# Optimization experiments

Hardware: AMD Instinct MI355X
Metric: run time of the kernel (lower is better)

The kernel has to match this reference:

```python
import jax, jax.numpy as jnp
import numpy as np

NUM_HEADS = 8
NUM_KV_HEADS = 2
HEAD_DIM = 64
EPS = 1e-6
ROPE_BASE = 10000.0


def rmsnorm(x, w):
    # x: (..., head_dim)
    var = jnp.mean(x * x, axis=-1, keepdims=True)
    return x * jax.lax.rsqrt(var + EPS) * w


def apply_rope(x):
    # x: (B, L, nH, hd); positions along L, standard rotate-half RoPE
    B, L, nH, hd = x.shape
    inv_freq = 1.0 / (ROPE_BASE ** (jnp.arange(0, hd, 2, dtype=jnp.float32) / hd))  # (hd/2,)
    ang = jnp.arange(L, dtype=jnp.float32)[:, None] * inv_freq[None, :]  # (L, hd/2)
    cos = jnp.concatenate([jnp.cos(ang), jnp.cos(ang)], axis=-1)[None, :, None, :]  # (1,L,1,hd)
    sin = jnp.concatenate([jnp.sin(ang), jnp.sin(ang)], axis=-1)[None, :, None, :]
    x1, x2 = jnp.split(x, 2, axis=-1)
    rot = jnp.concatenate([-x2, x1], axis=-1)
    return x * cos + rot * sin


def setup_inputs() -> dict:
    key = jax.random.key(0)
    ks = jax.random.split(key, 6)
    width = 512
    x = jax.random.normal(ks[0], (1, 16, 16, 16, width), dtype=jnp.float32)
    s = 1.0 / np.sqrt(width)
    Wq = jax.random.normal(ks[1], (width, width), dtype=jnp.float32) * s
    Wk = jax.random.normal(ks[2], (NUM_KV_HEADS * HEAD_DIM, width), dtype=jnp.float32) * s
    Wv = jax.random.normal(ks[3], (NUM_KV_HEADS * HEAD_DIM, width), dtype=jnp.float32) * s
    Wo = jax.random.normal(ks[4], (width, width), dtype=jnp.float32) * s
    q_norm_w = jnp.ones((HEAD_DIM,), dtype=jnp.float32)
    k_norm_w = jnp.ones((HEAD_DIM,), dtype=jnp.float32)
    return {"x": x, "Wq": Wq, "Wk": Wk, "Wv": Wv,
            "q_norm_w": q_norm_w, "k_norm_w": k_norm_w, "Wo": Wo}


def reference(x, Wq, Wk, Wv, q_norm_w, k_norm_w, Wo):
    B, H, W, D, C = x.shape
    L = H * W * D
    xf = x.reshape(B, L, C)
    q = (xf @ Wq.T).reshape(B, L, NUM_HEADS, HEAD_DIM)
    k = (xf @ Wk.T).reshape(B, L, NUM_KV_HEADS, HEAD_DIM)
    v = (xf @ Wv.T).reshape(B, L, NUM_KV_HEADS, HEAD_DIM)
    q = apply_rope(rmsnorm(q, q_norm_w))
    k = apply_rope(rmsnorm(k, k_norm_w))
    # (B, heads, L, hd)
    q = q.transpose(0, 2, 1, 3)
    k = k.transpose(0, 2, 1, 3)
    v = v.transpose(0, 2, 1, 3)
    repeats = NUM_HEADS // NUM_KV_HEADS
    if repeats > 1:
        k = jnp.repeat(k, repeats, axis=1)
        v = jnp.repeat(v, repeats, axis=1)
    scale = 1.0 / np.sqrt(HEAD_DIM)
    scores = jnp.einsum('bhqd,bhkd->bhqk', q, k) * scale
    attn = jax.nn.softmax(scores, axis=-1)
    out = jnp.einsum('bhqk,bhkd->bhqd', attn, v)
    out = out.transpose(0, 2, 1, 3).reshape(B, H, W, D, C)
    return out @ Wo.T
```

## Files before the change

kernel.cpp:

```cpp
#include <hip/hip_runtime.h>
#include <hip/hip_bf16.h>
#include <math.h>

#define L_SEQ 4096
#define CDIM  512
#define NH    8
#define NKV   2
#define HD    64
#define EPS   1e-6f
#define QSCALE 0.18033688011f
#define NSPLIT 4
#define KVSPAN (L_SEQ / NSPLIT)

using short8 = __attribute__((ext_vector_type(8))) short;
using f32x4  = __attribute__((ext_vector_type(4))) float;
using f32x16 = __attribute__((ext_vector_type(16))) float;
typedef unsigned short ushort_t;

__device__ __forceinline__ ushort_t f2bf(float f) {
    union { float f; unsigned u; } c; c.f = f;
    unsigned r = c.u + 0x7FFF + ((c.u >> 16) & 1);
    return (ushort_t)(r >> 16);
}
__device__ __forceinline__ float bf2f(ushort_t u) {
    union { unsigned u; float f; } c; c.u = ((unsigned)u) << 16;
    return c.f;
}

#define GLOAD_LDS16(g, l)                                                  \
    __builtin_amdgcn_global_load_lds(                                      \
        (const __attribute__((address_space(1))) unsigned int*)(g),        \
        (__attribute__((address_space(3))) unsigned int*)(l), 16, 0, 0)

__device__ __forceinline__ short8 lds_read8(const char* p) {
    return *reinterpret_cast<const short8*>(__builtin_assume_aligned(p, 16));
}

__device__ __forceinline__ unsigned pk_bf16(float lo, float hi) {
    const unsigned a = __float_as_uint(hi) + 0x8000u;
    const unsigned b = __float_as_uint(lo) + 0x8000u;
    return __builtin_amdgcn_perm(a, b, 0x07060302u);
}

__global__ __launch_bounds__(256) void cvt_bf16(const float* __restrict__ x,
                                                const float* __restrict__ wq,
                                                const float* __restrict__ wk,
                                                const float* __restrict__ wv,
                                                const float* __restrict__ wo,
                                                ushort_t* __restrict__ xb,
                                                ushort_t* __restrict__ wqb,
                                                ushort_t* __restrict__ wkb,
                                                ushort_t* __restrict__ wvb,
                                                ushort_t* __restrict__ wob) {
    const size_t i = ((size_t)blockIdx.x * 256 + threadIdx.x) << 2;
    const float* s; ushort_t* d; size_t o;
    if (i < 2097152)      { s = x;  d = xb;  o = i; }
    else if (i < 2359296) { s = wq; d = wqb; o = i - 2097152; }
    else if (i < 2424832) { s = wk; d = wkb; o = i - 2359296; }
    else if (i < 2490368) { s = wv; d = wvb; o = i - 2424832; }
    else                  { s = wo; d = wob; o = i - 2490368; }
    const float4 v = *reinterpret_cast<const float4*>(s + o);
    ushort_t r[4] = { f2bf(v.x), f2bf(v.y), f2bf(v.z), f2bf(v.w) };
    *reinterpret_cast<uint2*>(d + o) = *reinterpret_cast<const uint2*>(r);
}

template<bool OUT_BF16>
__global__ __launch_bounds__(256) void gemm_bf16_nt(const ushort_t* __restrict__ A,
                                                    const ushort_t* __restrict__ B,
                                                    void* __restrict__ Cv,
                                                    int M, int N, int K) {
    __shared__ short As[2][4096];
    __shared__ short Bs[2][4096];

    const int tid = threadIdx.x;
    const int w = tid >> 6, lane = tid & 63;
    const int g = lane >> 4, r16 = lane & 15;
    const int wr = w >> 1, wc = w & 1;
    const int m0 = blockIdx.y * 64, n0 = blockIdx.x * 64;
    const int r7sw = (r16 & 7) << 4;

    const int lrow = lane >> 3;
    const int swzb = ((lane & 7) ^ lrow) << 4;
    const int c0 = w * 2, c1 = w * 2 + 1;
    const size_t rowK2 = (size_t)K * 2;

    const char* agA = (const char*)A + (size_t)(m0 + c0 * 8 + lrow) * rowK2 + swzb;
    const char* agB = agA + 8 * rowK2;
    const char* bgA = (const char*)B + (size_t)(n0 + c0 * 8 + lrow) * rowK2 + swzb;
    const char* bgB = bgA + 8 * rowK2;

    GLOAD_LDS16(agA, (char*)As[0] + c0 * 1024);
    GLOAD_LDS16(agB, (char*)As[0] + c1 * 1024);
    GLOAD_LDS16(bgA, (char*)Bs[0] + c0 * 1024);
    GLOAD_LDS16(bgB, (char*)Bs[0] + c1 * 1024);
    __syncthreads();

    f32x4 acc[2][2] = {};
    const int NKIT = K >> 6;
    int cur = 0;
    for (int it = 0; it < NKIT; ++it) {
        if (it + 1 < NKIT) {
            const size_t ko = (size_t)(it + 1) * 128;
            char* ad = (char*)As[cur ^ 1];
            char* bd = (char*)Bs[cur ^ 1];
            GLOAD_LDS16(agA + ko, ad + c0 * 1024);
            GLOAD_LDS16(agB + ko, ad + c1 * 1024);
            GLOAD_LDS16(bgA + ko, bd + c0 * 1024);
            GLOAD_LDS16(bgB + ko, bd + c1 * 1024);
        }
        const char* at = (const char*)As[cur];
        const char* bt = (const char*)Bs[cur];

        short8 af[2][2], bfr[2][2];
#pragma unroll
        for (int t = 0; t < 2; ++t)
#pragma unroll
            for (int ks = 0; ks < 2; ++ks) {
                af[t][ks]  = lds_read8(at + (wr * 32 + t * 16 + r16) * 128
                                          + ((ks * 64 + g * 16) ^ r7sw));
                bfr[t][ks] = lds_read8(bt + (wc * 32 + t * 16 + r16) * 128
                                          + ((ks * 64 + g * 16) ^ r7sw));
            }
        __builtin_amdgcn_s_setprio(1);
#pragma unroll
        for (int tm = 0; tm < 2; ++tm)
#pragma unroll
            for (int tn = 0; tn < 2; ++tn)
#pragma unroll
                for (int ks = 0; ks < 2; ++ks)
                    acc[tm][tn] = __builtin_amdgcn_mfma_f32_16x16x32_bf16(
                        af[tm][ks], bfr[tn][ks], acc[tm][tn], 0, 0, 0);
        __builtin_amdgcn_s_setprio(0);

        __syncthreads();
        cur ^= 1;
    }

#pragma unroll
    for (int tm = 0; tm < 2; ++tm)
#pragma unroll
        for (int tn = 0; tn < 2; ++tn)
#pragma unroll
            for (int jj = 0; jj < 4; ++jj) {
                const int row = m0 + wr * 32 + tm * 16 + g * 4 + jj;
                const int col = n0 + wc * 32 + tn * 16 + r16;
                if (OUT_BF16)
                    ((ushort_t*)Cv)[(size_t)row * N + col] = f2bf(acc[tm][tn][jj]);
                else
                    ((float*)Cv)[(size_t)row * N + col] = acc[tm][tn][jj];
            }
}

__global__ __launch_bounds__(256) void norm_rope(ushort_t* __restrict__ q,
                                                 ushort_t* __restrict__ k,
                                                 const float* __restrict__ qw,
                                                 const float* __restrict__ kw) {
    const int wid  = threadIdx.x >> 6;
    const int lane = threadIdx.x & 63;
    const long row = (long)blockIdx.x * 4 + wid;
    const long QROWS = (long)L_SEQ * NH;

    ushort_t* ptr;
    const float* w;
    int pos;
    const bool isq = (row < QROWS);
    if (isq) {
        pos = (int)(row >> 3);
        ptr = q + (size_t)pos * (NH * HD) + (int)(row & 7) * HD;
        w = qw;
    } else {
        const long r = row - QROWS;
        pos = (int)(r >> 1);
        ptr = k + (size_t)pos * (NKV * HD) + (int)(r & 1) * HD;
        w = kw;
    }

    float x = bf2f(ptr[lane]);
    float ss = x * x;
#pragma unroll
    for (int off = 32; off; off >>= 1) ss += __shfl_xor(ss, off);
    float xn = x * rsqrtf(ss * (1.0f / 64.0f) + EPS) * w[lane];

    float xp = __shfl_xor(xn, 32);
    const int i = lane & 31;
    const float inv_freq = exp2f((float)i * -0.41524101186f);
    float s, c;
    sincosf((float)pos * inv_freq, &s, &c);
    float out = (lane < 32) ? (xn * c - xp * s) : (xn * c + xp * s);
    if (isq) out *= QSCALE;
    ptr[lane] = f2bf(out);
}

__global__ __launch_bounds__(256, 3) void attn_mfma(const ushort_t* __restrict__ qb,
                                                    const ushort_t* __restrict__ kb,
                                                    const ushort_t* __restrict__ vtb,
                                                    ushort_t* __restrict__ opart,
                                                    float* __restrict__ lpart) {
    __shared__ short Ks[2][4096];
    __shared__ short Vs[2][4096];

    const int tid = threadIdx.x;
    const int w = tid >> 6, lane = tid & 63;
    const int l31 = lane & 31, hf = lane >> 5;
    const int h = blockIdx.y, hkv = h >> 2;
    const int s = blockIdx.z;
    const int kvb = s * KVSPAN;
    const int qw = blockIdx.x * 128 + w * 32;
    const int swz = (lane & 7) << 4;
    const bool lo = (hf == 0);

    const int lrow = lane >> 3;
    const int swzb = ((lane & 7) ^ lrow) << 4;
    const int c0 = w * 2, c1 = w * 2 + 1;

    const char* kgA = (const char*)kb + (size_t)(kvb + c0 * 8 + lrow) * (NKV * HD * 2)
                      + hkv * (HD * 2) + swzb;
    const char* kgB = kgA + 8 * (NKV * HD * 2);
    const char* vgA = (const char*)vtb + (size_t)(hkv * HD + c0 * 8 + lrow) * (L_SEQ * 2)
                      + (size_t)kvb * 2 + swzb;
    const char* vgB = vgA + 8 * (size_t)(L_SEQ * 2);

    short8 qf[4];
#pragma unroll
    for (int ks = 0; ks < 4; ++ks)
        qf[ks] = *reinterpret_cast<const short8*>(
            &qb[(size_t)(qw + l31) * CDIM + h * HD + ks * 16 + hf * 8]);

    GLOAD_LDS16(kgA, (char*)Ks[0] + c0 * 1024);
    GLOAD_LDS16(kgB, (char*)Ks[0] + c1 * 1024);
    GLOAD_LDS16(vgA, (char*)Vs[0] + c0 * 1024);
    GLOAD_LDS16(vgB, (char*)Vs[0] + c1 * 1024);
    __syncthreads();

    f32x16 oacc[2] = {};
    float lsum = 0.0f;

    int cur = 0;
    for (int it = 0; it < KVSPAN / 64; ++it) {
        if (it + 1 < KVSPAN / 64) {
            const size_t ko = (size_t)(it + 1) * 64 * (NKV * HD * 2);
            const size_t vo = (size_t)(it + 1) * 128;
            char* kd = (char*)Ks[cur ^ 1];
            char* vd = (char*)Vs[cur ^ 1];
            GLOAD_LDS16(kgA + ko, kd + c0 * 1024);
            GLOAD_LDS16(kgB + ko, kd + c1 * 1024);
            GLOAD_LDS16(vgA + vo, vd + c0 * 1024);
            GLOAD_LDS16(vgB + vo, vd + c1 * 1024);
        }

        const char* kt = (const char*)Ks[cur];
        const char* vt = (const char*)Vs[cur];

        f32x16 sacc[2] = {};
        __builtin_amdgcn_s_setprio(1);
#pragma unroll
        for (int sub = 0; sub < 2; ++sub) {
#pragma unroll
            for (int ks = 0; ks < 4; ++ks) {
                const short8 kf = lds_read8(
                    kt + (sub * 32 + l31) * 128 + ((ks * 32 + hf * 16) ^ swz));
                sacc[sub] = __builtin_amdgcn_mfma_f32_32x32x16_bf16(
                    kf, qf[ks], sacc[sub], 0, 0, 0);
            }
        }
        __builtin_amdgcn_s_setprio(0);

        unsigned pkv[16];
#pragma unroll
        for (int sub = 0; sub < 2; ++sub) {
#pragma unroll
            for (int r2 = 0; r2 < 8; ++r2) {
                const float x = exp2f(sacc[sub][2 * r2]);
                const float y = exp2f(sacc[sub][2 * r2 + 1]);
                lsum += x + y;
                pkv[sub * 8 + r2] = pk_bf16(x, y);
            }
        }

        short8 pfrag[4];
#pragma unroll
        for (int kk = 0; kk < 4; ++kk) {
            const unsigned a0 = pkv[kk * 4 + 0], a1 = pkv[kk * 4 + 1];
            const unsigned b0 = pkv[kk * 4 + 2], b1 = pkv[kk * 4 + 3];
            const unsigned pa0 = __shfl_xor(a0, 32), pa1 = __shfl_xor(a1, 32);
            const unsigned pb0 = __shfl_xor(b0, 32), pb1 = __shfl_xor(b1, 32);
            union { unsigned u[4]; short8 s8; } pf;
            pf.u[0] = lo ? a0 : pb0;  pf.u[1] = lo ? a1 : pb1;
            pf.u[2] = lo ? pa0 : b0;  pf.u[3] = lo ? pa1 : b1;
            pfrag[kk] = pf.s8;
        }

        __builtin_amdgcn_s_setprio(1);
#pragma unroll
        for (int n = 0; n < 2; ++n) {
#pragma unroll
            for (int kk = 0; kk < 4; ++kk) {
                const short8 vf = lds_read8(
                    vt + (n * 32 + l31) * 128 + ((kk * 32 + hf * 16) ^ swz));
                oacc[n] = __builtin_amdgcn_mfma_f32_32x32x16_bf16(
                    pfrag[kk], vf, oacc[n], 0, 0, 0);
            }
        }
        __builtin_amdgcn_s_setprio(0);

        __syncthreads();
        cur ^= 1;
    }

    lsum += __shfl_xor(lsum, 32);
    ushort_t* op = opart + (size_t)s * L_SEQ * CDIM;
    float* lp = lpart + (size_t)s * L_SEQ * NH;
    if (lane < 32) lp[(size_t)(qw + lane) * NH + h] = lsum;
#pragma unroll
    for (int n = 0; n < 2; ++n)
#pragma unroll
        for (int r = 0; r < 16; ++r) {
            const int row = qw + (r & 3) + 8 * (r >> 2) + 4 * hf;
            const int col = h * HD + n * 32 + l31;
            op[(size_t)row * CDIM + col] = f2bf(oacc[n][r]);
        }
}

__global__ __launch_bounds__(256) void combine_splits(const ushort_t* __restrict__ opart,
                                                      const float* __restrict__ lpart,
                                                      ushort_t* __restrict__ out) {
    const size_t i4 = ((size_t)blockIdx.x * 256 + threadIdx.x) << 2;
    const int row = (int)(i4 >> 9);
    const int h = (int)((i4 & 511) >> 6);
    float l = 0.0f;
#pragma unroll
    for (int s = 0; s < NSPLIT; ++s)
        l += lpart[(size_t)s * L_SEQ * NH + (size_t)row * NH + h];
    const float inv = 1.0f / l;

    float acc[4] = {};
#pragma unroll
    for (int s = 0; s < NSPLIT; ++s) {
        ushort_t a[4];
        *reinterpret_cast<uint2*>(a) =
            *reinterpret_cast<const uint2*>(opart + (size_t)s * L_SEQ * CDIM + i4);
#pragma unroll
        for (int j = 0; j < 4; ++j) acc[j] += bf2f(a[j]);
    }
    ushort_t r[4];
#pragma unroll
    for (int j = 0; j < 4; ++j) r[j] = f2bf(acc[j] * inv);
    *reinterpret_cast<uint2*>(out + i4) = *reinterpret_cast<const uint2*>(r);
}

extern "C" void kernel_launch(void* const* d_in, const int* in_sizes, int n_in,
                              void* d_out, int out_size, void* d_ws, size_t ws_size,
                              hipStream_t stream) {
    const float* x   = (const float*)d_in[0];
    const float* Wq  = (const float*)d_in[1];
    const float* Wk  = (const float*)d_in[2];
    const float* Wv  = (const float*)d_in[3];
    const float* qnw = (const float*)d_in[4];
    const float* knw = (const float*)d_in[5];
    const float* Wo  = (const float*)d_in[6];
    float* out = (float*)d_out;

    char* p = (char*)d_ws;
    ushort_t* opart = (ushort_t*)p;
    ushort_t* xb    = opart;
    ushort_t* abuf  = opart;
    ushort_t* qbuf  = (ushort_t*)(p + (16u << 20));
    ushort_t* kbuf  = (ushort_t*)(p + (20u << 20));
    ushort_t* vtb   = (ushort_t*)(p + (21u << 20));
    ushort_t* wqb   = (ushort_t*)(p + (22u << 20));
    ushort_t* wkb   = wqb + (size_t)CDIM * CDIM;
    ushort_t* wvb   = wkb + (size_t)NKV * HD * CDIM;
    ushort_t* wob   = wvb + (size_t)NKV * HD * CDIM;
    float*    lpart = (float*)(wob + (size_t)CDIM * CDIM);

    const dim3 blk(256);

    cvt_bf16<<<dim3(2688), blk, 0, stream>>>(x, Wq, Wk, Wv, Wo, xb, wqb, wkb, wvb, wob);

    gemm_bf16_nt<true><<<dim3(8, 64),  blk, 0, stream>>>(xb, wqb, qbuf, L_SEQ, CDIM, CDIM);
    gemm_bf16_nt<true><<<dim3(2, 64),  blk, 0, stream>>>(xb, wkb, kbuf, L_SEQ, NKV * HD, CDIM);
    gemm_bf16_nt<true><<<dim3(64, 2),  blk, 0, stream>>>(wvb, xb, vtb, NKV * HD, L_SEQ, CDIM);

    norm_rope<<<dim3((L_SEQ * (NH + NKV)) / 4), blk, 0, stream>>>(qbuf, kbuf, qnw, knw);

    attn_mfma<<<dim3(L_SEQ / 128, NH, NSPLIT), blk, 0, stream>>>(qbuf, kbuf, vtb, opart, lpart);

    combine_splits<<<dim3((L_SEQ * CDIM) / (256 * 4)), blk, 0, stream>>>(opart, lpart, abuf);

    gemm_bf16_nt<false><<<dim3(8, 64), blk, 0, stream>>>(abuf, wob, out, L_SEQ, CDIM, CDIM);
}
```

Before: 108.5 us.

## Raise KV split count, compute row sums via MFMA, use permlane32 swap

The KV split count becomes a runtime value that rises to 8 when the workspace is large enough, and the workspace layout is repacked to fit it. Softmax row sums now come from an extra MFMA against a ones vector instead of scalar adds plus a shuffle reduction. The lane exchange for the P fragment uses permlane32_swap instead of four shuffles and selects, and bf16 packing switches to the HIP round-to-nearest intrinsic. Launch bounds rise to 4 blocks per CU and the score loop is restructured to lower register pressure. The extra MFMAs, the larger partial buffers and the heavier combine pass may offset the gain from more parallelism.

```diff
diff --git a/kernel.cpp b/kernel.cpp
--- a/kernel.cpp
+++ b/kernel.cpp
@@ -9,8 +9,6 @@
 #define HD    64
 #define EPS   1e-6f
 #define QSCALE 0.18033688011f
-#define NSPLIT 4
-#define KVSPAN (L_SEQ / NSPLIT)
 
 using short8 = __attribute__((ext_vector_type(8))) short;
 using f32x4  = __attribute__((ext_vector_type(4))) float;
@@ -37,9 +35,9 @@
 }
 
 __device__ __forceinline__ unsigned pk_bf16(float lo, float hi) {
-    const unsigned a = __float_as_uint(hi) + 0x8000u;
-    const unsigned b = __float_as_uint(lo) + 0x8000u;
-    return __builtin_amdgcn_perm(a, b, 0x07060302u);
+    const __hip_bfloat162 h2 = __float22bfloat162_rn(make_float2(lo, hi));
+    unsigned w; __builtin_memcpy(&w, &h2, 4);
+    return w;
 }
 
 __global__ __launch_bounds__(256) void cvt_bf16(const float* __restrict__ x,
@@ -191,7 +189,7 @@
     ptr[lane] = f2bf(out);
 }
 
-__global__ __launch_bounds__(256, 3) void attn_mfma(const ushort_t* __restrict__ qb,
+__global__ __launch_bounds__(256, 4) void attn_mfma(const ushort_t* __restrict__ qb,
                                                     const ushort_t* __restrict__ kb,
                                                     const ushort_t* __restrict__ vtb,
                                                     ushort_t* __restrict__ opart,
@@ -204,10 +202,10 @@
     const int l31 = lane & 31, hf = lane >> 5;
     const int h = blockIdx.y, hkv = h >> 2;
     const int s = blockIdx.z;
-    const int kvb = s * KVSPAN;
+    const int kvspan = L_SEQ / gridDim.z;
+    const int kvb = s * kvspan;
     const int qw = blockIdx.x * 128 + w * 32;
     const int swz = (lane & 7) << 4;
-    const bool lo = (hf == 0);
 
     const int lrow = lane >> 3;
     const int swzb = ((lane & 7) ^ lrow) << 4;
@@ -226,6 +224,12 @@
         qf[ks] = *reinterpret_cast<const short8*>(
             &qb[(size_t)(qw + l31) * CDIM + h * HD + ks * 16 + hf * 8]);
 
+    short8 onesf;
+    {
+        const short ob = (l31 == 0) ? (short)0x3F80 : (short)0;
+        onesf = short8{ob, ob, ob, ob, ob, ob, ob, ob};
+    }
+
     GLOAD_LDS16(kgA, (char*)Ks[0] + c0 * 1024);
     GLOAD_LDS16(kgB, (char*)Ks[0] + c1 * 1024);
     GLOAD_LDS16(vgA, (char*)Vs[0] + c0 * 1024);
@@ -233,11 +237,12 @@
     __syncthreads();
 
     f32x16 oacc[2] = {};
-    float lsum = 0.0f;
+    f32x16 oaccl = {};
 
     int cur = 0;
-    for (int it = 0; it < KVSPAN / 64; ++it) {
-        if (it + 1 < KVSPAN / 64) {
+    const int nit = kvspan >> 6;
+    for (int it = 0; it < nit; ++it) {
+        if (it + 1 < nit) {
             const size_t ko = (size_t)(it + 1) * 64 * (NKV * HD * 2);
             const size_t vo = (size_t)(it + 1) * 128;
             char* kd = (char*)Ks[cur ^ 1];
@@ -251,54 +256,44 @@
         const char* kt = (const char*)Ks[cur];
         const char* vt = (const char*)Vs[cur];
 
-        f32x16 sacc[2] = {};
-        __builtin_amdgcn_s_setprio(1);
+        unsigned pkv[16];
 #pragma unroll
         for (int sub = 0; sub < 2; ++sub) {
+            f32x16 sacc = {};
+            __builtin_amdgcn_s_setprio(1);
 #pragma unroll
             for (int ks = 0; ks < 4; ++ks) {
                 const short8 kf = lds_read8(
                     kt + (sub * 32 + l31) * 128 + ((ks * 32 + hf * 16) ^ swz));
-                sacc[sub] = __builtin_amdgcn_mfma_f32_32x32x16_bf16(
-                    kf, qf[ks], sacc[sub], 0, 0, 0);
+                sacc = __builtin_amdgcn_mfma_f32_32x32x16_bf16(kf, qf[ks], sacc, 0, 0, 0);
             }
-        }
-        __builtin_amdgcn_s_setprio(0);
-
-        unsigned pkv[16];
-#pragma unroll
-        for (int sub = 0; sub < 2; ++sub) {
-#pragma unroll
-            for (int r2 = 0; r2 < 8; ++r2) {
-                const float x = exp2f(sacc[sub][2 * r2]);
-                const float y = exp2f(sacc[sub][2 * r2 + 1]);
-                lsum += x + y;
-                pkv[sub * 8 + r2] = pk_bf16(x, y);
-            }
+            __builtin_amdgcn_s_setprio(0);
+#pragma unroll
+            for (int r2 = 0; r2 < 8; ++r2)
+                pkv[sub * 8 + r2] = pk_bf16(exp2f(sacc[2 * r2]), exp2f(sacc[2 * r2 + 1]));
         }
 
         short8 pfrag[4];
 #pragma unroll
         for (int kk = 0; kk < 4; ++kk) {
-            const unsigned a0 = pkv[kk * 4 + 0], a1 = pkv[kk * 4 + 1];
-            const unsigned b0 = pkv[kk * 4 + 2], b1 = pkv[kk * 4 + 3];
-            const unsigned pa0 = __shfl_xor(a0, 32), pa1 = __shfl_xor(a1, 32);
-            const unsigned pb0 = __shfl_xor(b0, 32), pb1 = __shfl_xor(b1, 32);
+            auto s0 = __builtin_amdgcn_permlane32_swap(pkv[kk * 4 + 0], pkv[kk * 4 + 2], false, false);
+            auto s1 = __builtin_amdgcn_permlane32_swap(pkv[kk * 4 + 1], pkv[kk * 4 + 3], false, false);
             union { unsigned u[4]; short8 s8; } pf;
-            pf.u[0] = lo ? a0 : pb0;  pf.u[1] = lo ? a1 : pb1;
-            pf.u[2] = lo ? pa0 : b0;  pf.u[3] = lo ? pa1 : b1;
+            pf.u[0] = s0[0]; pf.u[1] = s1[0]; pf.u[2] = s0[1]; pf.u[3] = s1[1];
             pfrag[kk] = pf.s8;
         }
 
         __builtin_amdgcn_s_setprio(1);
+#pragma unroll
+        for (int kk = 0; kk < 4; ++kk)
+            oaccl = __builtin_amdgcn_mfma_f32_32x32x16_bf16(pfrag[kk], onesf, oaccl, 0, 0, 0);
 #pragma unroll
         for (int n = 0; n < 2; ++n) {
 #pragma unroll
             for (int kk = 0; kk < 4; ++kk) {
                 const short8 vf = lds_read8(
                     vt + (n * 32 + l31) * 128 + ((kk * 32 + hf * 16) ^ swz));
-                oacc[n] = __builtin_amdgcn_mfma_f32_32x32x16_bf16(
-                    pfrag[kk], vf, oacc[n], 0, 0, 0);
+                oacc[n] = __builtin_amdgcn_mfma_f32_32x32x16_bf16(pfrag[kk], vf, oacc[n], 0, 0, 0);
             }
         }
         __builtin_amdgcn_s_setprio(0);
@@ -307,35 +302,38 @@
         cur ^= 1;
     }
 
-    lsum += __shfl_xor(lsum, 32);
     ushort_t* op = opart + (size_t)s * L_SEQ * CDIM;
-    float* lp = lpart + (size_t)s * L_SEQ * NH;
-    if (lane < 32) lp[(size_t)(qw + lane) * NH + h] = lsum;
 #pragma unroll
     for (int n = 0; n < 2; ++n)
 #pragma unroll
         for (int r = 0; r < 16; ++r) {
             const int row = qw + (r & 3) + 8 * (r >> 2) + 4 * hf;
-            const int col = h * HD + n * 32 + l31;
-            op[(size_t)row * CDIM + col] = f2bf(oacc[n][r]);
-        }
+            op[(size_t)row * CDIM + h * HD + n * 32 + l31] = f2bf(oacc[n][r]);
+        }
+    if (l31 == 0) {
+        float* lp = lpart + (size_t)s * L_SEQ * NH;
+#pragma unroll
+        for (int r = 0; r < 16; ++r) {
+            const int row = qw + (r & 3) + 8 * (r >> 2) + 4 * hf;
+            lp[(size_t)row * NH + h] = oaccl[r];
+        }
+    }
 }
 
 __global__ __launch_bounds__(256) void combine_splits(const ushort_t* __restrict__ opart,
                                                       const float* __restrict__ lpart,
-                                                      ushort_t* __restrict__ out) {
+                                                      ushort_t* __restrict__ out,
+                                                      int nsplit) {
     const size_t i4 = ((size_t)blockIdx.x * 256 + threadIdx.x) << 2;
     const int row = (int)(i4 >> 9);
     const int h = (int)((i4 & 511) >> 6);
     float l = 0.0f;
-#pragma unroll
-    for (int s = 0; s < NSPLIT; ++s)
+    for (int s = 0; s < nsplit; ++s)
         l += lpart[(size_t)s * L_SEQ * NH + (size_t)row * NH + h];
     const float inv = 1.0f / l;
 
     float acc[4] = {};
-#pragma unroll
-    for (int s = 0; s < NSPLIT; ++s) {
+    for (int s = 0; s < nsplit; ++s) {
         ushort_t a[4];
         *reinterpret_cast<uint2*>(a) =
             *reinterpret_cast<const uint2*>(opart + (size_t)s * L_SEQ * CDIM + i4);
@@ -360,17 +358,26 @@
     const float* Wo  = (const float*)d_in[6];
     float* out = (float*)d_out;
 
+    const size_t tail = (size_t)L_SEQ * CDIM * 2
+                      + (size_t)L_SEQ * NKV * HD * 2 * 2
+                      + (size_t)CDIM * CDIM * 2 * 2
+                      + (size_t)NKV * HD * CDIM * 2 * 2
+                      + (size_t)8 * L_SEQ * NH * 4;
+    const size_t need8 = (size_t)8 * L_SEQ * CDIM * 2 + tail;
+    const int nsplit = (ws_size >= need8) ? 8 : 4;
+
     char* p = (char*)d_ws;
     ushort_t* opart = (ushort_t*)p;
     ushort_t* xb    = opart;
     ushort_t* abuf  = opart;
-    ushort_t* qbuf  = (ushort_t*)(p + (16u << 20));
-    ushort_t* kbuf  = (ushort_t*)(p + (20u << 20));
-    ushort_t* vtb   = (ushort_t*)(p + (21u << 20));
-    ushort_t* wqb   = (ushort_t*)(p + (22u << 20));
-    ushort_t* wkb   = wqb + (size_t)CDIM * CDIM;
-    ushort_t* wvb   = wkb + (size_t)NKV * HD * CDIM;
-    ushort_t* wob   = wvb + (size_t)NKV * HD * CDIM;
+    char* q = p + (size_t)nsplit * L_SEQ * CDIM * 2;
+    ushort_t* qbuf = (ushort_t*)q;
+    ushort_t* kbuf = qbuf + (size_t)L_SEQ * CDIM;
+    ushort_t* vtb  = kbuf + (size_t)L_SEQ * NKV * HD;
+    ushort_t* wqb  = vtb  + (size_t)L_SEQ * NKV * HD;
+    ushort_t* wkb  = wqb  + (size_t)CDIM * CDIM;
+    ushort_t* wvb  = wkb  + (size_t)NKV * HD * CDIM;
+    ushort_t* wob  = wvb  + (size_t)NKV * HD * CDIM;
     float*    lpart = (float*)(wob + (size_t)CDIM * CDIM);
 
     const dim3 blk(256);
@@ -383,9 +390,9 @@
 
     norm_rope<<<dim3((L_SEQ * (NH + NKV)) / 4), blk, 0, stream>>>(qbuf, kbuf, qnw, knw);
 
-    attn_mfma<<<dim3(L_SEQ / 128, NH, NSPLIT), blk, 0, stream>>>(qbuf, kbuf, vtb, opart, lpart);
-
-    combine_splits<<<dim3((L_SEQ * CDIM) / (256 * 4)), blk, 0, stream>>>(opart, lpart, abuf);
+    attn_mfma<<<dim3(L_SEQ / 128, NH, nsplit), blk, 0, stream>>>(qbuf, kbuf, vtb, opart, lpart);
+
+    combine_splits<<<dim3((L_SEQ * CDIM) / (256 * 4)), blk, 0, stream>>>(opart, lpart, abuf, nsplit);
 
     gemm_bf16_nt<false><<<dim3(8, 64), blk, 0, stream>>>(abuf, wob, out, L_SEQ, CDIM, CDIM);
 }
```

After: 112.3 us. 3.6% more time.
